# Performance work log

Measured on AMD Instinct MI355X. Metric: run time of the kernel, lower is better.

The kernel has to match this reference:

```python
import jax, jax.numpy as jnp
import numpy as np

N, E, B, T, F, H, O = 50000, 800000, 16, 4, 128, 128, 128
LEAKY = 0.2  # PyG GATConv negative_slope default


def setup_inputs() -> dict:
    key = jax.random.key(0)
    ks = jax.random.split(key, 12)
    s = 0.05
    return {
        "x": jax.random.normal(ks[0], (T, N, F), jnp.float32),
        "edge_index": jax.random.randint(ks[1], (2, E), 0, N, dtype=jnp.int32),
        "batch_idx": jnp.sort(jax.random.randint(ks[2], (N,), 0, B, dtype=jnp.int32)),
        "W1": jax.random.normal(ks[3], (F, H), jnp.float32) * s,
        "att_src1": jax.random.normal(ks[4], (H,), jnp.float32) * s,
        "att_dst1": jax.random.normal(ks[5], (H,), jnp.float32) * s,
        "b1": jnp.zeros((H,), jnp.float32),
        "W2": jax.random.normal(ks[6], (H, O), jnp.float32) * s,
        "att_src2": jax.random.normal(ks[7], (O,), jnp.float32) * s,
        "att_dst2": jax.random.normal(ks[8], (O,), jnp.float32) * s,
        "b2": jnp.zeros((O,), jnp.float32),
    }


def gat_layer(h, src, dst, W, a_src, a_dst, b):
    # PyG GATConv, heads=1, concat=False, self-loops already appended.
    h = h @ W                                  # [N, out]
    alpha_s = h @ a_src                        # [N]
    alpha_d = h @ a_dst                        # [N]
    e = alpha_s[src] + alpha_d[dst]            # [E']
    e = jnp.where(e > 0, e, LEAKY * e)         # leaky_relu
    # softmax over incoming edges of each destination node (every node has a self-loop)
    m = jax.ops.segment_max(e, dst, num_segments=N)
    ex = jnp.exp(e - m[dst])
    z = jax.ops.segment_sum(ex, dst, num_segments=N)
    alpha = ex / z[dst]                        # [E']
    out = jax.ops.segment_sum(alpha[:, None] * h[src], dst, num_segments=N)
    return out + b


def reference(x, edge_index, batch_idx, W1, att_src1, att_dst1, b1, W2, att_src2, att_dst2, b2):
    loops = jnp.arange(N, dtype=edge_index.dtype)
    src = jnp.concatenate([edge_index[0], loops])  # add_self_loops (PyG default)
    dst = jnp.concatenate([edge_index[1], loops])
    ones = jnp.ones((N, 1), jnp.float32)
    cnt = jax.ops.segment_sum(ones, batch_idx, num_segments=B)  # [B,1]

    def per_snapshot(xt):
        h = gat_layer(xt, src, dst, W1, att_src1, att_dst1, b1)
        h = jax.nn.relu(h)                     # inter-layer ReLU (dropout=0, eval)
        h = gat_layer(h, src, dst, W2, att_src2, att_dst2, b2)
        return jax.ops.segment_sum(h, batch_idx, num_segments=B) / cnt  # mean pool [B,O]

    reps = jax.vmap(per_snapshot)(x)           # [T, B, O]
    return jnp.transpose(reps, (1, 0, 2))      # [B, T, O]
```

## Files before the change

kernel.cpp:

```cpp
#include <hip/hip_runtime.h>
#include <hip/hip_bf16.h>

#define LEAKY 0.2f

typedef __attribute__((ext_vector_type(8))) short bf16x8;
typedef __attribute__((ext_vector_type(4))) float f32x4;
typedef __attribute__((ext_vector_type(2))) float f32x2;


__global__ __launch_bounds__(256) void k_init(int* cnt, int* bstart, int n, int nb) {
    int i = blockIdx.x * 256 + threadIdx.x;
    if (i < n) cnt[i] = 1;
    if (i < nb) bstart[i] = n;
}

__global__ __launch_bounds__(256) void k_count(const int* __restrict__ dst, int* cnt, int e,
                                               const int* __restrict__ bidx, int* bstart, int n) {
    int i = blockIdx.x * 256 + threadIdx.x;
    if (i < e) atomicAdd(&cnt[dst[i]], 1);
    if (i < n) {
        int b = bidx[i];
        if (i == 0 || bidx[i - 1] != b) atomicMin(&bstart[b], i);
    }
}

__device__ inline int block_incl_scan(int v, int* lds) {
    int lane = threadIdx.x & 63, wid = threadIdx.x >> 6;
    int s = v;
#pragma unroll
    for (int o = 1; o < 64; o <<= 1) { int t = __shfl_up(s, o); if (lane >= o) s += t; }
    if (lane == 63) lds[wid] = s;
    __syncthreads();
    int add = 0;
#pragma unroll
    for (int ww = 0; ww < 3; ++ww) if (ww < wid) add += lds[ww];
    return s + add;
}

__global__ __launch_bounds__(256) void k_scanA(const int* __restrict__ cnt, int* bsum, int n) {
    __shared__ int lds[4];
    int i = blockIdx.x * 256 + threadIdx.x;
    int v = (i < n) ? ((cnt[i] + 15) & ~15) : 0;
    int s = block_incl_scan(v, lds);
    if (threadIdx.x == 255) bsum[blockIdx.x] = s;
}

__global__ __launch_bounds__(256) void k_scanB(int* bsum, int* boff, int nb,
                                               int* bstart, int n, int nbatch) {
    __shared__ int lds[4];
    int i = threadIdx.x;
    int v = (i < nb) ? bsum[i] : 0;
    int s = block_incl_scan(v, lds);
    if (i < nb) boff[i] = s - v;
    if (i == 0) {
        bstart[nbatch] = n;
        for (int b = nbatch - 1; b >= 0; --b)
            if (bstart[b] == n) bstart[b] = bstart[b + 1];
    }
}

__global__ __launch_bounds__(256) void k_scanC(const int* __restrict__ cnt, const int* __restrict__ boff,
                                               int* row_ptr, int* csr, int* cursor, int n) {
    __shared__ int lds[4];
    int i = blockIdx.x * 256 + threadIdx.x;
    int v = (i < n) ? ((cnt[i] + 15) & ~15) : 0;
    int s = block_incl_scan(v, lds) + boff[blockIdx.x];
    if (i < n) {
        int excl = s - v;
        row_ptr[i + 1] = s;
        csr[excl] = i;
        cursor[i] = excl + 1;
    }
    if (i == 0) row_ptr[0] = 0;
}

__global__ __launch_bounds__(256) void k_scatter(const int* __restrict__ src, const int* __restrict__ dst,
                                                 int* cursor, int* csr, int e) {
    int i = blockIdx.x * 256 + threadIdx.x;
    if (i < e) { int p = atomicAdd(&cursor[dst[i]], 1); csr[p] = src[i]; }
}

__global__ __launch_bounds__(256) void k_pad(const int* __restrict__ row_ptr, const int* __restrict__ cursor,
                                             int* csr, int n) {
    int i = blockIdx.x * 256 + threadIdx.x;
    if (i >= n) return;
    int p = cursor[i], e = row_ptr[i + 1];
    int v = i | 0x80000000;
    for (; p < e; ++p) csr[p] = v;
}

__device__ inline unsigned short bf16r(float x) {
    unsigned int u = __float_as_uint(x);
    u += 0x7fffu + ((u >> 16) & 1u);
    return (unsigned short)(u >> 16);
}

__device__ inline unsigned int bfpair(float lo, float hi) {
    unsigned int ul = __float_as_uint(lo); ul += 0x7fffu + ((ul >> 16) & 1u);
    unsigned int uh = __float_as_uint(hi); uh += 0x7fffu + ((uh >> 16) & 1u);
    return (ul >> 16) | (uh & 0xffff0000u);
}

template <bool ABF16>
__global__ __launch_bounds__(256) void k_gemm_mfma(
    const void* __restrict__ Asrc, const float* __restrict__ W,
    const float* __restrict__ asrc, const float* __restrict__ adst,
    unsigned char* __restrict__ hq, float* __restrict__ vas, float* __restrict__ vad,
    int nrows)
{
    __shared__ unsigned short Wt[128 * 136];
    int tid = threadIdx.x;
    int lane = tid & 63, wv = tid >> 6;
    int row0 = blockIdx.x * 128;
    int c0 = lane & 15, g = lane >> 4;

    {
        int k = tid >> 1;
        int n0 = (tid & 1) * 64;
        const float4* wr = (const float4*)&W[k * 128 + n0];
#pragma unroll
        for (int i = 0; i < 16; ++i) {
            float4 v = wr[i];
            int n = n0 + i * 4;
            Wt[(n + 0) * 136 + k] = bf16r(v.x);
            Wt[(n + 1) * 136 + k] = bf16r(v.y);
            Wt[(n + 2) * 136 + k] = bf16r(v.z);
            Wt[(n + 3) * 136 + k] = bf16r(v.w);
        }
    }
    __syncthreads();

    f32x4 acc[2][8];
#pragma unroll
    for (int mi = 0; mi < 2; ++mi)
#pragma unroll
        for (int ni = 0; ni < 8; ++ni)
#pragma unroll
            for (int q = 0; q < 4; ++q) acc[mi][ni][q] = 0.f;

    int rA[2];
#pragma unroll
    for (int mi = 0; mi < 2; ++mi)
        rA[mi] = min(row0 + wv * 32 + mi * 16 + c0, nrows - 1);

#pragma unroll
    for (int ks = 0; ks < 4; ++ks) {
        int k0 = ks * 32;
        bf16x8 af[2];
#pragma unroll
        for (int mi = 0; mi < 2; ++mi) {
            if (ABF16) {
                af[mi] = *(const bf16x8*)((const unsigned short*)Asrc + (size_t)rA[mi] * 128 + k0 + g * 8);
            } else {
                const float4* ap = (const float4*)((const float*)Asrc + (size_t)rA[mi] * 128 + k0 + g * 8);
                float4 f0 = ap[0], f1 = ap[1];
                uint4 p = make_uint4(bfpair(f0.x, f0.y), bfpair(f0.z, f0.w),
                                     bfpair(f1.x, f1.y), bfpair(f1.z, f1.w));
                af[mi] = *(bf16x8*)&p;
            }
        }
        bf16x8 bfr[8];
#pragma unroll
        for (int ni = 0; ni < 8; ++ni)
            bfr[ni] = *(const bf16x8*)&Wt[(ni * 16 + c0) * 136 + k0 + g * 8];
#pragma unroll
        for (int mi = 0; mi < 2; ++mi)
#pragma unroll
            for (int ni = 0; ni < 8; ++ni)
                acc[mi][ni] = __builtin_amdgcn_mfma_f32_16x16x32_bf16(af[mi], bfr[ni], acc[mi][ni], 0, 0, 0);
    }

    float as_s[8], ad_s[8];
#pragma unroll
    for (int ni = 0; ni < 8; ++ni) {
        as_s[ni] = asrc[ni * 16 + c0];
        ad_s[ni] = adst[ni * 16 + c0];
    }
#pragma unroll
    for (int mi = 0; mi < 2; ++mi) {
#pragma unroll
        for (int reg = 0; reg < 4; ++reg) {
            int row = row0 + wv * 32 + mi * 16 + g * 4 + reg;
            bool rowok = row < nrows;
            float v[8];
            float s = 0.f, d = 0.f;
#pragma unroll
            for (int ni = 0; ni < 8; ++ni) {
                v[ni] = acc[mi][ni][reg];
                s = fmaf(v[ni], as_s[ni], s);
                d = fmaf(v[ni], ad_s[ni], d);
            }
#pragma unroll
            for (int o = 1; o < 16; o <<= 1) { s += __shfl_xor(s, o); d += __shfl_xor(d, o); }
            if (rowok && c0 == 0) { vas[row] = s; vad[row] = d; }
#pragma unroll
            for (int ni = 0; ni < 8; ++ni) {
                float vn = __shfl_xor(v[ni], 1);
                unsigned int w = (unsigned int)__builtin_amdgcn_cvt_pk_fp8_f32(v[ni], vn, 0, false);
                if (rowok && (c0 & 1) == 0)
                    *(unsigned short*)&hq[(size_t)row * 128 + ni * 16 + c0] = (unsigned short)w;
            }
        }
    }
}

template <bool RELU>
__global__ __launch_bounds__(256) void k_agg(const unsigned char* __restrict__ hq,
                                             const float* __restrict__ vas,
                                             const float* __restrict__ vad,
                                             const int* __restrict__ row_ptr,
                                             const int* __restrict__ csr,
                                             const float* __restrict__ bias,
                                             unsigned int* __restrict__ outb,
                                             int n, int chunksPerT) {
    int i = blockIdx.x;
    int slot = i & 7;
    int t = slot >> 1;
    int chunk = ((i >> 3) << 1) | (slot & 1);
    if (chunk >= chunksPerT) return;
    int tid = threadIdx.x;
    int grp = tid >> 4, l = tid & 15;
    int w = chunk * 16 + grp;
    if (w >= n) return;
    unsigned int tbase = (unsigned int)t * (unsigned int)n;
    unsigned int g = tbase + (unsigned int)w;
    int beg = row_ptr[w], end = row_ptr[w + 1];
    float advl = vad[g];

    f32x2 acc2[4];
#pragma unroll
    for (int q = 0; q < 4; ++q) { acc2[q].x = 0.f; acc2[q].y = 0.f; }
    float zp = 0.f;

    for (int c = beg; c < end; c += 16) {
        int raw = csr[c + l];
        unsigned int s_l = tbase + (unsigned int)(raw & 0x7fffffff);
        float e = vas[s_l] + advl;
        e = e > 0.f ? e : LEAKY * e;
        float w_l = (raw >= 0) ? __expf(e) : 0.f;
        zp += w_l;

        unsigned int ofs[16]; float wt[16];
#pragma unroll
        for (int q = 0; q < 16; ++q) {
            ofs[q] = __shfl(s_l, q, 16) * 128u + (unsigned int)(l * 8);
            wt[q] = __shfl(w_l, q, 16);
        }
        uint2 v[16];
#pragma unroll
        for (int q = 0; q < 16; ++q)
            v[q] = *(const uint2*)&hq[ofs[q]];
#pragma unroll
        for (int q = 0; q < 16; ++q) {
            f32x2 w2; w2.x = wt[q]; w2.y = wt[q];
            acc2[0] = __builtin_elementwise_fma(w2, __builtin_amdgcn_cvt_pk_f32_fp8(v[q].x, false), acc2[0]);
            acc2[1] = __builtin_elementwise_fma(w2, __builtin_amdgcn_cvt_pk_f32_fp8(v[q].x, true),  acc2[1]);
            acc2[2] = __builtin_elementwise_fma(w2, __builtin_amdgcn_cvt_pk_f32_fp8(v[q].y, false), acc2[2]);
            acc2[3] = __builtin_elementwise_fma(w2, __builtin_amdgcn_cvt_pk_f32_fp8(v[q].y, true),  acc2[3]);
        }
    }

    float z = zp;
#pragma unroll
    for (int o = 1; o < 16; o <<= 1) z += __shfl_xor(z, o, 16);
    float inv = 1.0f / z;

    float4 b0 = *(const float4*)&bias[l * 8];
    float4 b1 = *(const float4*)&bias[l * 8 + 4];
    float4 o0 = make_float4(fmaf(acc2[0].x, inv, b0.x), fmaf(acc2[0].y, inv, b0.y),
                            fmaf(acc2[1].x, inv, b0.z), fmaf(acc2[1].y, inv, b0.w));
    float4 o1 = make_float4(fmaf(acc2[2].x, inv, b1.x), fmaf(acc2[2].y, inv, b1.y),
                            fmaf(acc2[3].x, inv, b1.z), fmaf(acc2[3].y, inv, b1.w));
    if (RELU) {
        o0.x = fmaxf(o0.x, 0.f); o0.y = fmaxf(o0.y, 0.f); o0.z = fmaxf(o0.z, 0.f); o0.w = fmaxf(o0.w, 0.f);
        o1.x = fmaxf(o1.x, 0.f); o1.y = fmaxf(o1.y, 0.f); o1.z = fmaxf(o1.z, 0.f); o1.w = fmaxf(o1.w, 0.f);
    }
    uint4 p = make_uint4(bfpair(o0.x, o0.y), bfpair(o0.z, o0.w),
                         bfpair(o1.x, o1.y), bfpair(o1.z, o1.w));
    *(uint4*)&outb[(size_t)g * 64 + l * 4] = p;
}

__global__ __launch_bounds__(128) void k_pool(const unsigned int* __restrict__ h,
                                              const int* __restrict__ bstart,
                                              float* __restrict__ out, int n, int T) {
    int b = blockIdx.x;
    int chunk = blockIdx.y;
    int t = blockIdx.z;
    int f = threadIdx.x;
    int s = bstart[b], e = bstart[b + 1];
    int cnt = e - s;
    if (cnt <= 0) return;
    int len = (cnt + 31) / 32;
    int cs = s + chunk * len;
    int ce = min(cs + len, e);
    if (cs >= ce) return;
    const unsigned int* ht = h + (size_t)t * n * 64;
    float acc = 0.f;
    for (int nidx = cs; nidx < ce; ++nidx) {
        unsigned int v = ht[(size_t)nidx * 64 + (f >> 1)];
        acc += __uint_as_float((f & 1) ? (v & 0xffff0000u) : (v << 16));
    }
    atomicAdd(&out[(size_t)(b * T + t) * 128 + f], acc / (float)cnt);
}


extern "C" void kernel_launch(void* const* d_in, const int* in_sizes, int n_in,
                              void* d_out, int out_size, void* d_ws, size_t ws_size,
                              hipStream_t stream) {
    const float* x    = (const float*)d_in[0];
    const int*   ei   = (const int*)d_in[1];
    const int*   bidx = (const int*)d_in[2];
    const float* W1   = (const float*)d_in[3];
    const float* as1  = (const float*)d_in[4];
    const float* ad1  = (const float*)d_in[5];
    const float* b1   = (const float*)d_in[6];
    const float* W2   = (const float*)d_in[7];
    const float* as2  = (const float*)d_in[8];
    const float* ad2  = (const float*)d_in[9];
    const float* b2   = (const float*)d_in[10];
    float* out = (float*)d_out;

    const int E = in_sizes[1] / 2;
    const int N = in_sizes[2];
    const int T = in_sizes[0] / (N * 128);
    const int B = out_size / (T * 128);
    const int* src = ei;
    const int* dst = ei + E;
    const int NT = N * T;

    char* wsp = (char*)d_ws;
    auto alloc = [&](size_t bytes) { void* p = wsp; wsp += (bytes + 255) / 256 * 256; return p; };
    unsigned char* hq    = (unsigned char*)alloc((size_t)NT * 128);
    unsigned int* hb2    = (unsigned int*)alloc((size_t)NT * 64 * 4);
    float* vas           = (float*)alloc((size_t)NT * 4);
    float* vad           = (float*)alloc((size_t)NT * 4);
    int* row_ptr         = (int*)alloc((size_t)(N + 1) * 4);
    int* cnt             = (int*)alloc((size_t)N * 4);
    int* csr             = (int*)alloc(((size_t)E + 16ull * N + 64) * 4);
    int* bstart          = (int*)alloc((size_t)(B + 2) * 4);
    int  nScanB          = (N + 255) / 256;
    int* bsum            = (int*)alloc((size_t)nScanB * 4);
    int* boff            = (int*)alloc((size_t)nScanB * 4);

    hipMemsetAsync(d_out, 0, (size_t)out_size * sizeof(float), stream);

    int gN = (N + 255) / 256, gE = (E + 255) / 256;
    k_init<<<gN, 256, 0, stream>>>(cnt, bstart, N, B + 1);
    k_count<<<gE, 256, 0, stream>>>(dst, cnt, E, bidx, bstart, N);
    k_scanA<<<nScanB, 256, 0, stream>>>(cnt, bsum, N);
    k_scanB<<<1, 256, 0, stream>>>(bsum, boff, nScanB, bstart, N, B);
    k_scanC<<<nScanB, 256, 0, stream>>>(cnt, boff, row_ptr, csr, cnt, N);
    k_scatter<<<gE, 256, 0, stream>>>(src, dst, cnt, csr, E);
    k_pad<<<gN, 256, 0, stream>>>(row_ptr, cnt, csr, N);

    int gGemm = (NT + 127) / 128;
    int chunksPerT = (N + 15) / 16;
    int chunksPad = ((chunksPerT + 1) / 2) * 2;
    int gAggFlat = chunksPad * 4;
    k_gemm_mfma<false><<<gGemm, 256, 0, stream>>>(x,   W1, as1, ad1, hq, vas, vad, NT);
    k_agg<true ><<<gAggFlat, 256, 0, stream>>>(hq, vas, vad, row_ptr, csr, b1, hb2, N, chunksPerT);
    k_gemm_mfma<true ><<<gGemm, 256, 0, stream>>>(hb2, W2, as2, ad2, hq, vas, vad, NT);
    k_agg<false><<<gAggFlat, 256, 0, stream>>>(hq, vas, vad, row_ptr, csr, b2, hb2, N, chunksPerT);
    k_pool<<<dim3(B, 32, T), 128, 0, stream>>>(hb2, bstart, out, N, T);
}
```

Measured before the change: 350.5 us.

## Precompute per-edge softmax weights in separate kernel, vectorize CSR and weight loads in aggregation

Adds a per-slot dst map, built in k_pad, and a new k_weights kernel. It computes the exp(leaky(as+ad)) edge weights for all four snapshots into a slot-major table before each aggregation. k_agg then reads 16 CSR indices and 16 weights as int4/float4 vectors per lane instead of gathering vas per lane and broadcasting with shuffles. This also drops the z cross-lane reduction, since every lane now sums all 16 weights itself. The cost is two extra launches and roughly 4x slots x 4 bytes of extra weight-table writes and reads, plus the dstOf array.

```diff
diff --git a/kernel.cpp b/kernel.cpp
--- a/kernel.cpp
+++ b/kernel.cpp
@@ -81,12 +81,33 @@
 }
 
 __global__ __launch_bounds__(256) void k_pad(const int* __restrict__ row_ptr, const int* __restrict__ cursor,
-                                             int* csr, int n) {
+                                             int* csr, int* dstOf, int n) {
     int i = blockIdx.x * 256 + threadIdx.x;
     if (i >= n) return;
-    int p = cursor[i], e = row_ptr[i + 1];
+    int b0 = row_ptr[i], p = cursor[i], e = row_ptr[i + 1];
+    for (int s = b0; s < e; ++s) dstOf[s] = i;
     int v = i | 0x80000000;
     for (; p < e; ++p) csr[p] = v;
+}
+
+__global__ __launch_bounds__(256) void k_weights(const int* __restrict__ csr,
+                                                 const int* __restrict__ dstOf,
+                                                 const float* __restrict__ vas,
+                                                 const float* __restrict__ vad,
+                                                 const int* __restrict__ row_ptrN,
+                                                 float* __restrict__ wts, int n, int slotsCap) {
+    int s = blockIdx.x * 256 + threadIdx.x;
+    if (s >= row_ptrN[0]) return;
+    int raw = csr[s];
+    int srcn = raw & 0x7fffffff;
+    int d = dstOf[s];
+#pragma unroll
+    for (int t = 0; t < 4; ++t) {
+        int tb = t * n;
+        float e = vas[tb + srcn] + vad[tb + d];
+        e = e > 0.f ? e : LEAKY * e;
+        wts[(size_t)t * slotsCap + s] = (raw >= 0) ? __expf(e) : 0.f;
+    }
 }
 
 __device__ inline unsigned short bf16r(float x) {
@@ -206,13 +227,12 @@
 
 template <bool RELU>
 __global__ __launch_bounds__(256) void k_agg(const unsigned char* __restrict__ hq,
-                                             const float* __restrict__ vas,
-                                             const float* __restrict__ vad,
+                                             const float* __restrict__ wts,
                                              const int* __restrict__ row_ptr,
                                              const int* __restrict__ csr,
                                              const float* __restrict__ bias,
                                              unsigned int* __restrict__ outb,
-                                             int n, int chunksPerT) {
+                                             int n, int chunksPerT, int slotsCap) {
     int i = blockIdx.x;
     int slot = i & 7;
     int t = slot >> 1;
@@ -225,45 +245,45 @@
     unsigned int tbase = (unsigned int)t * (unsigned int)n;
     unsigned int g = tbase + (unsigned int)w;
     int beg = row_ptr[w], end = row_ptr[w + 1];
-    float advl = vad[g];
+    const float* wtab = wts + (size_t)t * slotsCap;
+    unsigned l8 = (unsigned)(l * 8);
 
     f32x2 acc2[4];
 #pragma unroll
     for (int q = 0; q < 4; ++q) { acc2[q].x = 0.f; acc2[q].y = 0.f; }
     float zp = 0.f;
 
+#define FMA16(V, WT)                                                           \
+    {                                                                          \
+        _Pragma("unroll") for (int q = 0; q < 16; ++q) {                       \
+            f32x2 w2; w2.x = WT[q]; w2.y = WT[q];                              \
+            acc2[0] = __builtin_elementwise_fma(w2, __builtin_amdgcn_cvt_pk_f32_fp8(V[q].x, false), acc2[0]); \
+            acc2[1] = __builtin_elementwise_fma(w2, __builtin_amdgcn_cvt_pk_f32_fp8(V[q].x, true),  acc2[1]); \
+            acc2[2] = __builtin_elementwise_fma(w2, __builtin_amdgcn_cvt_pk_f32_fp8(V[q].y, false), acc2[2]); \
+            acc2[3] = __builtin_elementwise_fma(w2, __builtin_amdgcn_cvt_pk_f32_fp8(V[q].y, true),  acc2[3]); \
+        }                                                                      \
+    }
+
     for (int c = beg; c < end; c += 16) {
-        int raw = csr[c + l];
-        unsigned int s_l = tbase + (unsigned int)(raw & 0x7fffffff);
-        float e = vas[s_l] + advl;
-        e = e > 0.f ? e : LEAKY * e;
-        float w_l = (raw >= 0) ? __expf(e) : 0.f;
-        zp += w_l;
-
-        unsigned int ofs[16]; float wt[16];
-#pragma unroll
-        for (int q = 0; q < 16; ++q) {
-            ofs[q] = __shfl(s_l, q, 16) * 128u + (unsigned int)(l * 8);
-            wt[q] = __shfl(w_l, q, 16);
-        }
+        const int4* cp4 = (const int4*)&csr[c];
+        int4 sA = cp4[0], sB = cp4[1], sC = cp4[2], sD = cp4[3];
+        const float4* wp4 = (const float4*)&wtab[c];
+        float4 wA = wp4[0], wB = wp4[1], wC = wp4[2], wD = wp4[3];
+        zp += ((wA.x + wA.y) + (wA.z + wA.w)) + ((wB.x + wB.y) + (wB.z + wB.w))
+            + ((wC.x + wC.y) + (wC.z + wC.w)) + ((wD.x + wD.y) + (wD.z + wD.w));
+        int ss[16] = { sA.x, sA.y, sA.z, sA.w, sB.x, sB.y, sB.z, sB.w,
+                       sC.x, sC.y, sC.z, sC.w, sD.x, sD.y, sD.z, sD.w };
+        float wt[16] = { wA.x, wA.y, wA.z, wA.w, wB.x, wB.y, wB.z, wB.w,
+                         wC.x, wC.y, wC.z, wC.w, wD.x, wD.y, wD.z, wD.w };
         uint2 v[16];
 #pragma unroll
         for (int q = 0; q < 16; ++q)
-            v[q] = *(const uint2*)&hq[ofs[q]];
-#pragma unroll
-        for (int q = 0; q < 16; ++q) {
-            f32x2 w2; w2.x = wt[q]; w2.y = wt[q];
-            acc2[0] = __builtin_elementwise_fma(w2, __builtin_amdgcn_cvt_pk_f32_fp8(v[q].x, false), acc2[0]);
-            acc2[1] = __builtin_elementwise_fma(w2, __builtin_amdgcn_cvt_pk_f32_fp8(v[q].x, true),  acc2[1]);
-            acc2[2] = __builtin_elementwise_fma(w2, __builtin_amdgcn_cvt_pk_f32_fp8(v[q].y, false), acc2[2]);
-            acc2[3] = __builtin_elementwise_fma(w2, __builtin_amdgcn_cvt_pk_f32_fp8(v[q].y, true),  acc2[3]);
-        }
-    }
-
-    float z = zp;
-#pragma unroll
-    for (int o = 1; o < 16; o <<= 1) z += __shfl_xor(z, o, 16);
-    float inv = 1.0f / z;
+            v[q] = *(const uint2*)&hq[(tbase + ((unsigned)ss[q] & 0x7fffffffu)) * 128u + l8];
+        FMA16(v, wt)
+    }
+#undef FMA16
+
+    float inv = 1.0f / zp;
 
     float4 b0 = *(const float4*)&bias[l * 8];
     float4 b1 = *(const float4*)&bias[l * 8 + 4];
@@ -327,6 +347,7 @@
     const int* src = ei;
     const int* dst = ei + E;
     const int NT = N * T;
+    const int slotsCap = (int)((((size_t)E + 16ull * N + 64 + 255) / 256) * 256);
 
     char* wsp = (char*)d_ws;
     auto alloc = [&](size_t bytes) { void* p = wsp; wsp += (bytes + 255) / 256 * 256; return p; };
@@ -336,7 +357,9 @@
     float* vad           = (float*)alloc((size_t)NT * 4);
     int* row_ptr         = (int*)alloc((size_t)(N + 1) * 4);
     int* cnt             = (int*)alloc((size_t)N * 4);
-    int* csr             = (int*)alloc(((size_t)E + 16ull * N + 64) * 4);
+    int* csr             = (int*)alloc((size_t)slotsCap * 4);
+    int* dstOf           = (int*)alloc((size_t)slotsCap * 4);
+    float* wts           = (float*)alloc((size_t)slotsCap * 4 * 4);
     int* bstart          = (int*)alloc((size_t)(B + 2) * 4);
     int  nScanB          = (N + 255) / 256;
     int* bsum            = (int*)alloc((size_t)nScanB * 4);
@@ -351,15 +374,18 @@
     k_scanB<<<1, 256, 0, stream>>>(bsum, boff, nScanB, bstart, N, B);
     k_scanC<<<nScanB, 256, 0, stream>>>(cnt, boff, row_ptr, csr, cnt, N);
     k_scatter<<<gE, 256, 0, stream>>>(src, dst, cnt, csr, E);
-    k_pad<<<gN, 256, 0, stream>>>(row_ptr, cnt, csr, N);
+    k_pad<<<gN, 256, 0, stream>>>(row_ptr, cnt, csr, dstOf, N);
 
     int gGemm = (NT + 127) / 128;
+    int gSlots = slotsCap / 256;
     int chunksPerT = (N + 15) / 16;
     int chunksPad = ((chunksPerT + 1) / 2) * 2;
     int gAggFlat = chunksPad * 4;
     k_gemm_mfma<false><<<gGemm, 256, 0, stream>>>(x,   W1, as1, ad1, hq, vas, vad, NT);
-    k_agg<true ><<<gAggFlat, 256, 0, stream>>>(hq, vas, vad, row_ptr, csr, b1, hb2, N, chunksPerT);
+    k_weights<<<gSlots, 256, 0, stream>>>(csr, dstOf, vas, vad, row_ptr + N, wts, N, slotsCap);
+    k_agg<true ><<<gAggFlat, 256, 0, stream>>>(hq, wts, row_ptr, csr, b1, hb2, N, chunksPerT, slotsCap);
     k_gemm_mfma<true ><<<gGemm, 256, 0, stream>>>(hb2, W2, as2, ad2, hq, vas, vad, NT);
-    k_agg<false><<<gAggFlat, 256, 0, stream>>>(hq, vas, vad, row_ptr, csr, b2, hb2, N, chunksPerT);
+    k_weights<<<gSlots, 256, 0, stream>>>(csr, dstOf, vas, vad, row_ptr + N, wts, N, slotsCap);
+    k_agg<false><<<gAggFlat, 256, 0, stream>>>(hq, wts, row_ptr, csr, b2, hb2, N, chunksPerT, slotsCap);
     k_pool<<<dim3(B, 32, T), 128, 0, stream>>>(hb2, bstart, out, N, T);
 }
```

New measurement: 399.6 us. +14.0%, slower.
